# Kernel tuning notes

Measured on AMD Instinct MI355X. Metric: run time of the kernel, lower is better.

The kernel has to match this reference:

```python
import jax, jax.numpy as jnp
import numpy as np

N = 200000
C = 128
B = 4
HF, WF = 32, 88
IMG_H, IMG_W = 256, 704
STRIDE = 8
MAX_BEV_RANGE = 54.0
HID = max(C // 2, 32)
LN_EPS = 1e-5


def setup_inputs() -> dict:
    key = jax.random.key(0)
    ks = jax.random.split(key, 16)
    x = jax.random.normal(ks[0], (N, C), jnp.float32)
    bid = jax.random.randint(ks[1], (N, 1), 0, B)
    zi = jax.random.randint(ks[2], (N, 1), 0, 5)
    yi = jax.random.randint(ks[3], (N, 1), 0, 180)
    xi = jax.random.randint(ks[4], (N, 1), 0, 180)
    indices = jnp.concatenate([bid, zi, yi, xi], axis=1).astype(jnp.int32)
    voxel_size = jnp.array([0.075, 0.075, 0.2], jnp.float32)
    pc_range = jnp.array([-54.0, -54.0, -5.0, 54.0, 54.0, 3.0], jnp.float32)
    aug = jnp.tile(jnp.eye(4, dtype=jnp.float32)[None], (B, 1, 1)) + 0.01 * jax.random.normal(ks[5], (B, 4, 4), jnp.float32)
    # realistic pinhole lidar->image projection (depth = lidar +x)
    trans_base = np.array([[352.0, -560.0, 0.0, 0.0],
                           [128.0, 0.0, -560.0, 0.0],
                           [1.0, 0.0, 0.0, 0.0]], np.float32)
    trans = jnp.asarray(trans_base)[None] + 0.01 * jax.random.normal(ks[6], (B, 3, 4), jnp.float32)
    img_feats = jax.random.normal(ks[7], (B, C, HF, WF), jnp.float32)
    s = 0.05
    return {
        'x': x, 'indices': indices, 'voxel_size': voxel_size, 'pc_range': pc_range,
        'lidar_aug_matrix': aug, 'trans_lidar_to_img': trans, 'img_feats': img_feats,
        'W1_fg': s * jax.random.normal(ks[8], (C, HID), jnp.float32),
        'b1_fg': jnp.zeros((HID,), jnp.float32),
        'W2_fg': s * jax.random.normal(ks[9], (HID, 1), jnp.float32),
        'b2_fg': jnp.zeros((1,), jnp.float32),
        'We1': s * jax.random.normal(ks[10], (2 * C, C), jnp.float32),
        'be1': jnp.zeros((C,), jnp.float32),
        'We2': s * jax.random.normal(ks[11], (C, C), jnp.float32),
        'be2': jnp.zeros((C,), jnp.float32),
        'ln_gamma': jnp.ones((C,), jnp.float32),
        'ln_beta': jnp.zeros((C,), jnp.float32),
        'img_h': IMG_H, 'img_w': IMG_W,
    }


def _bilinear_gather(img_feats, batch_ids, u_norm, v_norm):
    # F.grid_sample(align_corners=True, padding_mode='zeros'), batched via per-point gather
    _, _, H, W = img_feats.shape
    xp = (u_norm + 1.0) * 0.5 * (W - 1)
    yp = (v_norm + 1.0) * 0.5 * (H - 1)
    x0 = jnp.floor(xp)
    y0 = jnp.floor(yp)
    wx1 = xp - x0
    wy1 = yp - y0

    def corner(xi, yi):
        ok = (xi >= 0) & (xi <= W - 1) & (yi >= 0) & (yi <= H - 1)
        xc = jnp.clip(xi, 0, W - 1).astype(jnp.int32)
        yc = jnp.clip(yi, 0, H - 1).astype(jnp.int32)
        return img_feats[batch_ids, :, yc, xc] * ok[:, None]  # [N, C]

    f00 = corner(x0, y0)
    f01 = corner(x0 + 1, y0)
    f10 = corner(x0, y0 + 1)
    f11 = corner(x0 + 1, y0 + 1)
    w00 = ((1 - wx1) * (1 - wy1))[:, None]
    w01 = (wx1 * (1 - wy1))[:, None]
    w10 = ((1 - wx1) * wy1)[:, None]
    w11 = (wx1 * wy1)[:, None]
    return w00 * f00 + w01 * f01 + w10 * f10 + w11 * f11


def reference(x, indices, voxel_size, pc_range, lidar_aug_matrix, trans_lidar_to_img, img_feats,
              W1_fg, b1_fg, W2_fg, b2_fg, We1, be1, We2, be2, ln_gamma, ln_beta, img_h, img_w):
    bids = indices[:, 0].astype(jnp.int32)
    # voxel centers: indices cols (z,y,x) -> (x,y,z)
    spatial = indices[:, jnp.array([3, 2, 1])].astype(jnp.float32)
    cvs = voxel_size * STRIDE
    centers = spatial * cvs + pc_range[:3] + cvs * 0.5  # [N, 3]
    range_norm = jnp.linalg.norm(centers[:, :2], axis=-1, keepdims=True)
    range_norm = jnp.clip(range_norm / max(MAX_BEV_RANGE, 1e-6), 0.0, 1.0)

    xyz_hom = jnp.concatenate([centers, jnp.ones((centers.shape[0], 1), centers.dtype)], axis=1)
    aug_inv = jnp.linalg.inv(lidar_aug_matrix)[bids]  # [N, 4, 4]
    xyz_hom = jnp.einsum('nij,nj->ni', aug_inv, xyz_hom)
    pts = jnp.einsum('nij,nj->ni', trans_lidar_to_img[bids], xyz_hom)  # [N, 3]
    depth = pts[:, 2]
    safe_depth = jnp.maximum(depth, 1e-5)
    u_img = pts[:, 0] / safe_depth
    v_img = pts[:, 1] / safe_depth
    Hf, Wf = img_feats.shape[2], img_feats.shape[3]
    u_norm = 2.0 * (u_img * (float(Wf) / float(img_w))) / max(Wf - 1, 1) - 1.0
    v_norm = 2.0 * (v_img * (float(Hf) / float(img_h))) / max(Hf - 1, 1) - 1.0
    valid = (depth > 1e-5) & (jnp.abs(u_norm) <= 1.0) & (jnp.abs(v_norm) <= 1.0)  # [N]
    valid_f = valid.astype(x.dtype)[:, None]

    sampled_img = _bilinear_gather(img_feats, bids, u_norm, v_norm)  # [N, C]

    # ForegroundHead
    p_fg = jax.nn.sigmoid(jax.nn.relu(x @ W1_fg + b1_fg) @ W2_fg + b2_fg)
    # ConventionalFusionExpert with projection-valid mask
    h = jax.nn.relu(jnp.concatenate([x, sampled_img], axis=-1) @ We1 + be1)
    delta = (h @ We2 + be2) * valid_f

    gain = jnp.linalg.norm(delta, axis=-1, keepdims=True) / (jnp.linalg.norm(x, axis=-1, keepdims=True) + 1e-6)
    fusion_gain = jnp.clip(1.0 - jnp.exp(-gain), 0.0, 1.0)

    xr = x + delta
    mu = jnp.mean(xr, axis=-1, keepdims=True)
    var = jnp.mean(jnp.square(xr - mu), axis=-1, keepdims=True)
    x_out = (xr - mu) * jax.lax.rsqrt(var + LN_EPS) * ln_gamma + ln_beta

    return (x_out, p_fg, fusion_gain, range_norm, valid_f)
```

## Files before the change

kernel.cpp:

```cpp
#include <hip/hip_runtime.h>
#include <math.h>

#define CD  128
#define HFD 32
#define WFD 88

typedef __attribute__((ext_vector_type(4))) float  f4;
typedef __attribute__((ext_vector_type(8))) __bf16 b8;

__device__ __forceinline__ f4 mfma16(b8 a, b8 b, f4 c) {
  return __builtin_amdgcn_mfma_f32_16x16x32_bf16(a, b, c, 0, 0, 0);
}

__global__ void prep_inv_kernel(const float* __restrict__ aug,
                                float* __restrict__ auginv, int B) {
  int b = threadIdx.x;
  if (b >= B) return;
  double m[4][8];
  for (int i = 0; i < 4; ++i)
    for (int j = 0; j < 4; ++j) {
      m[i][j]     = (double)aug[b * 16 + i * 4 + j];
      m[i][4 + j] = (i == j) ? 1.0 : 0.0;
    }
  for (int col = 0; col < 4; ++col) {
    int piv = col;
    double best = fabs(m[col][col]);
    for (int r = col + 1; r < 4; ++r) {
      double v = fabs(m[r][col]);
      if (v > best) { best = v; piv = r; }
    }
    if (piv != col)
      for (int j = 0; j < 8; ++j) {
        double t = m[col][j]; m[col][j] = m[piv][j]; m[piv][j] = t;
      }
    double f = 1.0 / m[col][col];
    for (int j = 0; j < 8; ++j) m[col][j] *= f;
    for (int r = 0; r < 4; ++r)
      if (r != col) {
        double gg = m[r][col];
        for (int j = 0; j < 8; ++j) m[r][j] -= gg * m[col][j];
      }
  }
  for (int i = 0; i < 4; ++i)
    for (int j = 0; j < 4; ++j)
      auginv[b * 16 + i * 4 + j] = (float)m[i][4 + j];
}

__global__ void transpose_img_kernel(const float* __restrict__ img,
                                     __bf16* __restrict__ imgT, int total) {
  int o = blockIdx.x * blockDim.x + threadIdx.x;
  if (o >= total) return;
  int c   = o & (CD - 1);
  int pos = o >> 7;
  int xw  = pos % WFD;
  int tmp = pos / WFD;
  int yh  = tmp & (HFD - 1);
  int b   = tmp >> 5;
  imgT[o] = (__bf16)img[((b * CD + c) * HFD + yh) * WFD + xw];
}

__global__ void pack_weights_kernel(const float* __restrict__ W1,
                                    const float* __restrict__ We1,
                                    const float* __restrict__ We2,
                                    short* __restrict__ W1t,
                                    short* __restrict__ We1t,
                                    short* __restrict__ We2t) {
  int i = blockIdx.x * 256 + threadIdx.x;
  const float* W; short* O; int KB, Nw, idx; bool cmap;
  if (i < 8192)       { W = W1;  O = W1t;  KB = 4; Nw = 64;  idx = i;         cmap = true;  }
  else if (i < 40960) { W = We1; O = We1t; KB = 8; Nw = 128; idx = i - 8192;  cmap = true;  }
  else if (i < 57344) { W = We2; O = We2t; KB = 4; Nw = 128; idx = i - 40960; cmap = false; }
  else return;
  const int j    = idx & 7;
  const int lane = (idx >> 3) & 63;
  const int blk  = idx >> 9;
  const int kb   = blk % KB, mb = blk / KB;
  const int ch   = 16 * mb + (lane & 15);
  const int k    = cmap ? (32 * kb + 8 * (lane >> 4) + j)
                        : (32 * kb + 4 * (lane >> 4) + (j & 3) + 16 * (j >> 2));
  __bf16 h = (__bf16)W[k * Nw + ch];
  short s;
  __builtin_memcpy(&s, &h, 2);
  O[idx] = s;
}

__device__ __forceinline__ void geo_cat(
    int nc, int g, const float* __restrict__ x,
    const int* __restrict__ indices, const __bf16* __restrict__ imgT,
    const float* __restrict__ auginv, const float* __restrict__ trans,
    float vsx, float vsy, float vsz, float pcx, float pcy, float pcz,
    float su, float sv, b8* catf, float& vf_o, float& rn_o) {
  const int4 idx = *reinterpret_cast<const int4*>(indices + (size_t)nc * 4);
  const int  b   = idx.x;
  const float cx = (float)idx.w * vsx + pcx + 0.5f * vsx;
  const float cy = (float)idx.z * vsy + pcy + 0.5f * vsy;
  const float cz = (float)idx.y * vsz + pcz + 0.5f * vsz;

  const f4 A0 = *reinterpret_cast<const f4*>(auginv + b * 16 + 0);
  const f4 A1 = *reinterpret_cast<const f4*>(auginv + b * 16 + 4);
  const f4 A2 = *reinterpret_cast<const f4*>(auginv + b * 16 + 8);
  const f4 A3 = *reinterpret_cast<const f4*>(auginv + b * 16 + 12);
  const float h0 = A0[0] * cx + A0[1] * cy + A0[2] * cz + A0[3];
  const float h1 = A1[0] * cx + A1[1] * cy + A1[2] * cz + A1[3];
  const float h2 = A2[0] * cx + A2[1] * cy + A2[2] * cz + A2[3];
  const float h3 = A3[0] * cx + A3[1] * cy + A3[2] * cz + A3[3];
  const f4 T0 = *reinterpret_cast<const f4*>(trans + b * 12 + 0);
  const f4 T1 = *reinterpret_cast<const f4*>(trans + b * 12 + 4);
  const f4 T2 = *reinterpret_cast<const f4*>(trans + b * 12 + 8);
  const float q0    = T0[0] * h0 + T0[1] * h1 + T0[2] * h2 + T0[3] * h3;
  const float q1    = T1[0] * h0 + T1[1] * h1 + T1[2] * h2 + T1[3] * h3;
  const float depth = T2[0] * h0 + T2[1] * h1 + T2[2] * h2 + T2[3] * h3;
  const float safe  = fmaxf(depth, 1e-5f);
  const float u = q0 / safe, v = q1 / safe;
  const float un = 2.0f * (u * su) / 87.0f - 1.0f;
  const float vn = 2.0f * (v * sv) / 31.0f - 1.0f;
  vf_o = (depth > 1e-5f && fabsf(un) <= 1.0f && fabsf(vn) <= 1.0f) ? 1.0f : 0.0f;
  float rn = sqrtf(cx * cx + cy * cy) / 54.0f;
  rn_o = fminf(fmaxf(rn, 0.0f), 1.0f);

  const float xp  = (un + 1.0f) * 0.5f * 87.0f;
  const float yp  = (vn + 1.0f) * 0.5f * 31.0f;
  const float x0f = floorf(xp), y0f = floorf(yp);
  const float wx1 = xp - x0f, wy1 = yp - y0f;
  const float wx0 = 1.0f - wx1, wy0 = 1.0f - wy1;
  const bool okx0 = (x0f >= 0.0f) && (x0f <= 87.0f);
  const bool okx1 = (x0f + 1.0f >= 0.0f) && (x0f + 1.0f <= 87.0f);
  const bool oky0 = (y0f >= 0.0f) && (y0f <= 31.0f);
  const bool oky1 = (y0f + 1.0f >= 0.0f) && (y0f + 1.0f <= 31.0f);
  const int ix0 = (int)fminf(fmaxf(x0f, 0.0f), 87.0f);
  const int ix1 = (int)fminf(fmaxf(x0f + 1.0f, 0.0f), 87.0f);
  const int iy0 = (int)fminf(fmaxf(y0f, 0.0f), 31.0f);
  const int iy1 = (int)fminf(fmaxf(y0f + 1.0f, 0.0f), 31.0f);
  const float w00 = (okx0 && oky0) ? (wx0 * wy0) : 0.0f;
  const float w01 = (okx1 && oky0) ? (wx1 * wy0) : 0.0f;
  const float w10 = (okx0 && oky1) ? (wx0 * wy1) : 0.0f;
  const float w11 = (okx1 && oky1) ? (wx1 * wy1) : 0.0f;
  const int o00 = (iy0 * WFD + ix0) * CD;
  const int o01 = (iy0 * WFD + ix1) * CD;
  const int o10 = (iy1 * WFD + ix0) * CD;
  const int o11 = (iy1 * WFD + ix1) * CD;
  const __bf16* ib = imgT + (size_t)b * (HFD * WFD * CD);

  const float* xr = x + (size_t)nc * CD + 8 * g;
#pragma unroll
  for (int kb = 0; kb < 4; ++kb) {
    const f4 a = *reinterpret_cast<const f4*>(xr + 32 * kb);
    const f4 c = *reinterpret_cast<const f4*>(xr + 32 * kb + 4);
    b8 t;
#pragma unroll
    for (int e = 0; e < 4; ++e) {
      t[e]     = (__bf16)a[e];
      t[4 + e] = (__bf16)c[e];
    }
    catf[kb] = t;
  }
#pragma unroll
  for (int kb = 0; kb < 4; ++kb) {
    const int off = 32 * kb + 8 * g;
    const b8 f00 = *reinterpret_cast<const b8*>(ib + o00 + off);
    const b8 f01 = *reinterpret_cast<const b8*>(ib + o01 + off);
    const b8 f10 = *reinterpret_cast<const b8*>(ib + o10 + off);
    const b8 f11 = *reinterpret_cast<const b8*>(ib + o11 + off);
    b8 t;
#pragma unroll
    for (int e = 0; e < 8; ++e) {
      const float s = w00 * (float)f00[e] + w01 * (float)f01[e] +
                      w10 * (float)f10[e] + w11 * (float)f11[e];
      t[e] = (__bf16)s;
    }
    catf[4 + kb] = t;
  }
}

__device__ __forceinline__ void epilogue_pt(
    const f4* acc3, float vf, float rn, float sfg, int n, int nc, int g, int N,
    const float* __restrict__ x, const float* __restrict__ lng,
    const float* __restrict__ lnb, const float* __restrict__ b2,
    float* __restrict__ out, size_t OFF_PFG, size_t OFF_GAIN, size_t OFF_RN,
    size_t OFF_VAL) {
  f4 xrv[8];
  float sd = 0.0f, sx2 = 0.0f, sr = 0.0f, sr2 = 0.0f;
#pragma unroll
  for (int mb = 0; mb < 8; ++mb) {
    const f4 xv = *reinterpret_cast<const f4*>(x + (size_t)nc * CD + 16 * mb + 4 * g);
    const f4 d  = acc3[mb] * vf;
    const f4 r  = xv + d;
    xrv[mb] = r;
#pragma unroll
    for (int e = 0; e < 4; ++e) {
      sd  += d[e] * d[e];
      sx2 += xv[e] * xv[e];
      sr  += r[e];
      sr2 += r[e] * r[e];
    }
  }
  sd  += __shfl_xor(sd, 16);  sd  += __shfl_xor(sd, 32);
  sx2 += __shfl_xor(sx2, 16); sx2 += __shfl_xor(sx2, 32);
  sr  += __shfl_xor(sr, 16);  sr  += __shfl_xor(sr, 32);
  sr2 += __shfl_xor(sr2, 16); sr2 += __shfl_xor(sr2, 32);

  const float mu   = sr * (1.0f / 128.0f);
  const float var  = sr2 * (1.0f / 128.0f) - mu * mu;
  const float rstd = rsqrtf(var + 1e-5f);
  const float gn   = sqrtf(sd) / (sqrtf(sx2) + 1e-6f);
  const float fgain = fminf(fmaxf(1.0f - expf(-gn), 0.0f), 1.0f);

  if (n < N) {
#pragma unroll
    for (int mb = 0; mb < 8; ++mb) {
      const f4 gm = *reinterpret_cast<const f4*>(lng + 16 * mb + 4 * g);
      const f4 bt = *reinterpret_cast<const f4*>(lnb + 16 * mb + 4 * g);
      const f4 o  = (xrv[mb] - mu) * rstd * gm + bt;
      *reinterpret_cast<f4*>(out + (size_t)n * CD + 16 * mb + 4 * g) = o;
    }
    if (g == 0) {
      out[OFF_PFG  + n] = 1.0f / (1.0f + expf(-(sfg + b2[0])));
      out[OFF_GAIN + n] = fgain;
      out[OFF_RN   + n] = rn;
      out[OFF_VAL  + n] = vf;
    }
  }
}

__global__ __launch_bounds__(256)
void fused_mfma_kernel(const float* __restrict__ x,
                       const int* __restrict__ indices,
                       const float* __restrict__ voxel_size,
                       const float* __restrict__ pc_range,
                       const float* __restrict__ trans,
                       const float* __restrict__ auginv,
                       const __bf16* __restrict__ imgT,
                       const __bf16* __restrict__ W1t,
                       const float* __restrict__ b1,
                       const float* __restrict__ W2,
                       const float* __restrict__ b2,
                       const __bf16* __restrict__ We1t,
                       const float* __restrict__ be1,
                       const __bf16* __restrict__ We2t,
                       const float* __restrict__ be2,
                       const float* __restrict__ lng,
                       const float* __restrict__ lnb,
                       const int* __restrict__ img_h_p,
                       const int* __restrict__ img_w_p,
                       float* __restrict__ out, int N) {
  const int lane = threadIdx.x & 63;
  const int wv   = threadIdx.x >> 6;
  const int g    = lane >> 4;
  const int pl   = lane & 15;
  const int n0   = blockIdx.x * 128 + wv * 32 + pl;
  const int n1   = n0 + 16;
  const int nc0  = (n0 < N) ? n0 : (N - 1);
  const int nc1  = (n1 < N) ? n1 : (N - 1);

  const size_t NN       = (size_t)N;
  const size_t OFF_PFG  = NN * CD;
  const size_t OFF_GAIN = OFF_PFG + NN;
  const size_t OFF_RN   = OFF_GAIN + NN;
  const size_t OFF_VAL  = OFF_RN + NN;

  const float vsx = voxel_size[0] * 8.0f;
  const float vsy = voxel_size[1] * 8.0f;
  const float vsz = voxel_size[2] * 8.0f;
  const float pcx = pc_range[0], pcy = pc_range[1], pcz = pc_range[2];
  const float su  = (float)WFD / (float)(*img_w_p);
  const float sv  = (float)HFD / (float)(*img_h_p);

  b8 cat0[8], cat1[8];
  float vf0, rn0, vf1, rn1;
  geo_cat(nc0, g, x, indices, imgT, auginv, trans, vsx, vsy, vsz,
          pcx, pcy, pcz, su, sv, cat0, vf0, rn0);
  geo_cat(nc1, g, x, indices, imgT, auginv, trans, vsx, vsy, vsz,
          pcx, pcy, pcz, su, sv, cat1, vf1, rn1);

  float sfg0 = 0.0f, sfg1 = 0.0f;
#pragma unroll
  for (int mb = 0; mb < 4; ++mb) {
    const f4 bi = *reinterpret_cast<const f4*>(b1 + 16 * mb + 4 * g);
    f4 a0 = bi, a1 = bi;
#pragma unroll
    for (int kb = 0; kb < 4; ++kb) {
      const b8 w = *reinterpret_cast<const b8*>(
          W1t + ((size_t)(mb * 4 + kb) * 64 + lane) * 8);
      a0 = mfma16(w, cat0[kb], a0);
      a1 = mfma16(w, cat1[kb], a1);
    }
    const f4 w2v = *reinterpret_cast<const f4*>(W2 + 16 * mb + 4 * g);
#pragma unroll
    for (int e = 0; e < 4; ++e) {
      sfg0 += fmaxf(a0[e], 0.0f) * w2v[e];
      sfg1 += fmaxf(a1[e], 0.0f) * w2v[e];
    }
  }
  sfg0 += __shfl_xor(sfg0, 16); sfg0 += __shfl_xor(sfg0, 32);
  sfg1 += __shfl_xor(sfg1, 16); sfg1 += __shfl_xor(sfg1, 32);

  b8 b30[4], b31[4];
#pragma unroll
  for (int pr = 0; pr < 4; ++pr) {
    const f4 biA = *reinterpret_cast<const f4*>(be1 + 16 * (2 * pr) + 4 * g);
    const f4 biB = *reinterpret_cast<const f4*>(be1 + 16 * (2 * pr + 1) + 4 * g);
    f4 aA0 = biA, aB0 = biB, aA1 = biA, aB1 = biB;
#pragma unroll
    for (int kb = 0; kb < 8; ++kb) {
      const b8 wA = *reinterpret_cast<const b8*>(
          We1t + ((size_t)((2 * pr) * 8 + kb) * 64 + lane) * 8);
      const b8 wB = *reinterpret_cast<const b8*>(
          We1t + ((size_t)((2 * pr + 1) * 8 + kb) * 64 + lane) * 8);
      aA0 = mfma16(wA, cat0[kb], aA0);
      aB0 = mfma16(wB, cat0[kb], aB0);
      aA1 = mfma16(wA, cat1[kb], aA1);
      aB1 = mfma16(wB, cat1[kb], aB1);
    }
    b8 t0, t1;
#pragma unroll
    for (int e = 0; e < 4; ++e) {
      t0[e]     = (__bf16)fmaxf(aA0[e], 0.0f);
      t0[4 + e] = (__bf16)fmaxf(aB0[e], 0.0f);
      t1[e]     = (__bf16)fmaxf(aA1[e], 0.0f);
      t1[4 + e] = (__bf16)fmaxf(aB1[e], 0.0f);
    }
    b30[pr] = t0;
    b31[pr] = t1;
  }

  f4 acc30[8], acc31[8];
#pragma unroll
  for (int mb = 0; mb < 8; ++mb) {
    const f4 bi = *reinterpret_cast<const f4*>(be2 + 16 * mb + 4 * g);
    acc30[mb] = bi;
    acc31[mb] = bi;
  }
#pragma unroll
  for (int kb = 0; kb < 4; ++kb) {
#pragma unroll
    for (int mb = 0; mb < 8; ++mb) {
      const b8 w = *reinterpret_cast<const b8*>(
          We2t + ((size_t)(mb * 4 + kb) * 64 + lane) * 8);
      acc30[mb] = mfma16(w, b30[kb], acc30[mb]);
      acc31[mb] = mfma16(w, b31[kb], acc31[mb]);
    }
  }

  epilogue_pt(acc30, vf0, rn0, sfg0, n0, nc0, g, N, x, lng, lnb, b2, out,
              OFF_PFG, OFF_GAIN, OFF_RN, OFF_VAL);
  epilogue_pt(acc31, vf1, rn1, sfg1, n1, nc1, g, N, x, lng, lnb, b2, out,
              OFF_PFG, OFF_GAIN, OFF_RN, OFF_VAL);
}

extern "C" void kernel_launch(void* const* d_in, const int* in_sizes, int n_in,
                              void* d_out, int out_size, void* d_ws, size_t ws_size,
                              hipStream_t stream) {
  const float* x       = (const float*)d_in[0];
  const int*   indices = (const int*)d_in[1];
  const float* voxel   = (const float*)d_in[2];
  const float* pcr     = (const float*)d_in[3];
  const float* aug     = (const float*)d_in[4];
  const float* trans   = (const float*)d_in[5];
  const float* img     = (const float*)d_in[6];
  const float* W1      = (const float*)d_in[7];
  const float* b1      = (const float*)d_in[8];
  const float* W2      = (const float*)d_in[9];
  const float* b2      = (const float*)d_in[10];
  const float* We1     = (const float*)d_in[11];
  const float* be1     = (const float*)d_in[12];
  const float* We2     = (const float*)d_in[13];
  const float* be2     = (const float*)d_in[14];
  const float* lng     = (const float*)d_in[15];
  const float* lnb     = (const float*)d_in[16];
  const int*   img_h   = (const int*)d_in[17];
  const int*   img_w   = (const int*)d_in[18];

  const int N         = in_sizes[0] / CD;
  const int B         = in_sizes[4] / 16;
  const int img_total = in_sizes[6];
  const size_t IMG_BYTES = (size_t)img_total * 2;

  char*   wsb    = (char*)d_ws;
  float*  auginv = (float*)wsb;
  __bf16* imgT   = (__bf16*)(wsb + 1024);
  short*  W1t    = (short*)(wsb + 1024 + IMG_BYTES);
  short*  We1t   = W1t + 8192;
  short*  We2t   = We1t + 32768;

  prep_inv_kernel<<<1, 64, 0, stream>>>(aug, auginv, B);
  transpose_img_kernel<<<(img_total + 255) / 256, 256, 0, stream>>>(
      img, imgT, img_total);
  pack_weights_kernel<<<224, 256, 0, stream>>>(W1, We1, We2, W1t, We1t, We2t);
  fused_mfma_kernel<<<(N + 127) / 128, 256, 0, stream>>>(
      x, indices, voxel, pcr, trans, auginv, imgT,
      (const __bf16*)W1t, b1, W2, b2,
      (const __bf16*)We1t, be1,
      (const __bf16*)We2t, be2,
      lng, lnb, img_h, img_w, (float*)d_out, N);
}
```

Before: 133.6 us.

## Stage packed MLP weights in LDS and use 768-thread blocks with one point-tile per wave

The fused kernel now copies all packed bf16 weights (W1, We1, We2, about 112 KB) into shared memory at block start, and the MFMA loops read weight fragments from LDS instead of global memory. Blocks grow to 768 threads covering 192 points, with each wave handling a single 16-point tile instead of two, which lowers register pressure. The aim is to cut repeated global/L2 weight traffic and raise occupancy. The cost is a large per-block LDS fill plus a barrier, and 112 KB of LDS per block limits how many blocks fit on each CU.

```diff
diff --git a/kernel.cpp b/kernel.cpp
--- a/kernel.cpp
+++ b/kernel.cpp
@@ -222,7 +222,7 @@
   }
 }
 
-__global__ __launch_bounds__(256)
+__global__ __launch_bounds__(768)
 void fused_mfma_kernel(const float* __restrict__ x,
                        const int* __restrict__ indices,
                        const float* __restrict__ voxel_size,
@@ -230,33 +230,49 @@
                        const float* __restrict__ trans,
                        const float* __restrict__ auginv,
                        const __bf16* __restrict__ imgT,
-                       const __bf16* __restrict__ W1t,
+                       const short* __restrict__ wsrc,
                        const float* __restrict__ b1,
                        const float* __restrict__ W2,
                        const float* __restrict__ b2,
-                       const __bf16* __restrict__ We1t,
                        const float* __restrict__ be1,
-                       const __bf16* __restrict__ We2t,
                        const float* __restrict__ be2,
                        const float* __restrict__ lng,
                        const float* __restrict__ lnb,
                        const int* __restrict__ img_h_p,
                        const int* __restrict__ img_w_p,
                        float* __restrict__ out, int N) {
-  const int lane = threadIdx.x & 63;
-  const int wv   = threadIdx.x >> 6;
+  __shared__ __align__(16) short wlds[57344];
+  const int tid  = threadIdx.x;
+  const int lane = tid & 63;
+  const int wv   = tid >> 6;
   const int g    = lane >> 4;
   const int pl   = lane & 15;
-  const int n0   = blockIdx.x * 128 + wv * 32 + pl;
-  const int n1   = n0 + 16;
-  const int nc0  = (n0 < N) ? n0 : (N - 1);
-  const int nc1  = (n1 < N) ? n1 : (N - 1);
+  const int n    = blockIdx.x * 192 + wv * 16 + pl;
+  const int nc   = (n < N) ? n : (N - 1);
 
   const size_t NN       = (size_t)N;
   const size_t OFF_PFG  = NN * CD;
   const size_t OFF_GAIN = OFF_PFG + NN;
   const size_t OFF_RN   = OFF_GAIN + NN;
   const size_t OFF_VAL  = OFF_RN + NN;
+
+  {
+    const uint4* ws4 = reinterpret_cast<const uint4*>(wsrc);
+    uint4* wl4       = reinterpret_cast<uint4*>(wlds);
+    uint4 tmp[10];
+#pragma unroll
+    for (int i = 0; i < 10; ++i) {
+      int c = tid + i * 768;
+      if (c >= 7168) c -= 7168;
+      tmp[i] = ws4[c];
+    }
+#pragma unroll
+    for (int i = 0; i < 10; ++i) {
+      int c = tid + i * 768;
+      if (c >= 7168) c -= 7168;
+      wl4[c] = tmp[i];
+    }
+  }
 
   const float vsx = voxel_size[0] * 8.0f;
   const float vsy = voxel_size[1] * 8.0f;
@@ -265,85 +281,66 @@
   const float su  = (float)WFD / (float)(*img_w_p);
   const float sv  = (float)HFD / (float)(*img_h_p);
 
-  b8 cat0[8], cat1[8];
-  float vf0, rn0, vf1, rn1;
-  geo_cat(nc0, g, x, indices, imgT, auginv, trans, vsx, vsy, vsz,
-          pcx, pcy, pcz, su, sv, cat0, vf0, rn0);
-  geo_cat(nc1, g, x, indices, imgT, auginv, trans, vsx, vsy, vsz,
-          pcx, pcy, pcz, su, sv, cat1, vf1, rn1);
-
-  float sfg0 = 0.0f, sfg1 = 0.0f;
+  b8 cat[8];
+  float vf, rn;
+  geo_cat(nc, g, x, indices, imgT, auginv, trans, vsx, vsy, vsz,
+          pcx, pcy, pcz, su, sv, cat, vf, rn);
+
+  __syncthreads();
+
+  const short* wb = wlds + lane * 8;
+
+  float sfg = 0.0f;
 #pragma unroll
   for (int mb = 0; mb < 4; ++mb) {
-    const f4 bi = *reinterpret_cast<const f4*>(b1 + 16 * mb + 4 * g);
-    f4 a0 = bi, a1 = bi;
+    f4 a = *reinterpret_cast<const f4*>(b1 + 16 * mb + 4 * g);
 #pragma unroll
     for (int kb = 0; kb < 4; ++kb) {
-      const b8 w = *reinterpret_cast<const b8*>(
-          W1t + ((size_t)(mb * 4 + kb) * 64 + lane) * 8);
-      a0 = mfma16(w, cat0[kb], a0);
-      a1 = mfma16(w, cat1[kb], a1);
+      const b8 w = *reinterpret_cast<const b8*>(wb + (mb * 4 + kb) * 512);
+      a = mfma16(w, cat[kb], a);
     }
     const f4 w2v = *reinterpret_cast<const f4*>(W2 + 16 * mb + 4 * g);
 #pragma unroll
+    for (int e = 0; e < 4; ++e) sfg += fmaxf(a[e], 0.0f) * w2v[e];
+  }
+  sfg += __shfl_xor(sfg, 16);
+  sfg += __shfl_xor(sfg, 32);
+
+  b8 b3[4];
+#pragma unroll
+  for (int pr = 0; pr < 4; ++pr) {
+    f4 aA = *reinterpret_cast<const f4*>(be1 + 16 * (2 * pr) + 4 * g);
+    f4 aB = *reinterpret_cast<const f4*>(be1 + 16 * (2 * pr + 1) + 4 * g);
+#pragma unroll
+    for (int kb = 0; kb < 8; ++kb) {
+      const b8 wA = *reinterpret_cast<const b8*>(wb + (16 + (2 * pr) * 8 + kb) * 512);
+      const b8 wB = *reinterpret_cast<const b8*>(wb + (16 + (2 * pr + 1) * 8 + kb) * 512);
+      aA = mfma16(wA, cat[kb], aA);
+      aB = mfma16(wB, cat[kb], aB);
+    }
+    b8 t;
+#pragma unroll
     for (int e = 0; e < 4; ++e) {
-      sfg0 += fmaxf(a0[e], 0.0f) * w2v[e];
-      sfg1 += fmaxf(a1[e], 0.0f) * w2v[e];
-    }
-  }
-  sfg0 += __shfl_xor(sfg0, 16); sfg0 += __shfl_xor(sfg0, 32);
-  sfg1 += __shfl_xor(sfg1, 16); sfg1 += __shfl_xor(sfg1, 32);
-
-  b8 b30[4], b31[4];
-#pragma unroll
-  for (int pr = 0; pr < 4; ++pr) {
-    const f4 biA = *reinterpret_cast<const f4*>(be1 + 16 * (2 * pr) + 4 * g);
-    const f4 biB = *reinterpret_cast<const f4*>(be1 + 16 * (2 * pr + 1) + 4 * g);
-    f4 aA0 = biA, aB0 = biB, aA1 = biA, aB1 = biB;
-#pragma unroll
-    for (int kb = 0; kb < 8; ++kb) {
-      const b8 wA = *reinterpret_cast<const b8*>(
-          We1t + ((size_t)((2 * pr) * 8 + kb) * 64 + lane) * 8);
-      const b8 wB = *reinterpret_cast<const b8*>(
-          We1t + ((size_t)((2 * pr + 1) * 8 + kb) * 64 + lane) * 8);
-      aA0 = mfma16(wA, cat0[kb], aA0);
-      aB0 = mfma16(wB, cat0[kb], aB0);
-      aA1 = mfma16(wA, cat1[kb], aA1);
-      aB1 = mfma16(wB, cat1[kb], aB1);
-    }
-    b8 t0, t1;
-#pragma unroll
-    for (int e = 0; e < 4; ++e) {
-      t0[e]     = (__bf16)fmaxf(aA0[e], 0.0f);
-      t0[4 + e] = (__bf16)fmaxf(aB0[e], 0.0f);
-      t1[e]     = (__bf16)fmaxf(aA1[e], 0.0f);
-      t1[4 + e] = (__bf16)fmaxf(aB1[e], 0.0f);
-    }
-    b30[pr] = t0;
-    b31[pr] = t1;
-  }
-
-  f4 acc30[8], acc31[8];
-#pragma unroll
-  for (int mb = 0; mb < 8; ++mb) {
-    const f4 bi = *reinterpret_cast<const f4*>(be2 + 16 * mb + 4 * g);
-    acc30[mb] = bi;
-    acc31[mb] = bi;
-  }
+      t[e]     = (__bf16)fmaxf(aA[e], 0.0f);
+      t[4 + e] = (__bf16)fmaxf(aB[e], 0.0f);
+    }
+    b3[pr] = t;
+  }
+
+  f4 acc3[8];
+#pragma unroll
+  for (int mb = 0; mb < 8; ++mb)
+    acc3[mb] = *reinterpret_cast<const f4*>(be2 + 16 * mb + 4 * g);
 #pragma unroll
   for (int kb = 0; kb < 4; ++kb) {
 #pragma unroll
     for (int mb = 0; mb < 8; ++mb) {
-      const b8 w = *reinterpret_cast<const b8*>(
-          We2t + ((size_t)(mb * 4 + kb) * 64 + lane) * 8);
-      acc30[mb] = mfma16(w, b30[kb], acc30[mb]);
-      acc31[mb] = mfma16(w, b31[kb], acc31[mb]);
-    }
-  }
-
-  epilogue_pt(acc30, vf0, rn0, sfg0, n0, nc0, g, N, x, lng, lnb, b2, out,
-              OFF_PFG, OFF_GAIN, OFF_RN, OFF_VAL);
-  epilogue_pt(acc31, vf1, rn1, sfg1, n1, nc1, g, N, x, lng, lnb, b2, out,
+      const b8 w = *reinterpret_cast<const b8*>(wb + (80 + mb * 4 + kb) * 512);
+      acc3[mb] = mfma16(w, b3[kb], acc3[mb]);
+    }
+  }
+
+  epilogue_pt(acc3, vf, rn, sfg, n, nc, g, N, x, lng, lnb, b2, out,
               OFF_PFG, OFF_GAIN, OFF_RN, OFF_VAL);
 }
 
@@ -386,10 +383,8 @@
   transpose_img_kernel<<<(img_total + 255) / 256, 256, 0, stream>>>(
       img, imgT, img_total);
   pack_weights_kernel<<<224, 256, 0, stream>>>(W1, We1, We2, W1t, We1t, We2t);
-  fused_mfma_kernel<<<(N + 127) / 128, 256, 0, stream>>>(
+  fused_mfma_kernel<<<(N + 191) / 192, 768, 0, stream>>>(
       x, indices, voxel, pcr, trans, auginv, imgT,
-      (const __bf16*)W1t, b1, W2, b2,
-      (const __bf16*)We1t, be1,
-      (const __bf16*)We2t, be2,
+      W1t, b1, W2, b2, be1, be2,
       lng, lnb, img_h, img_w, (float*)d_out, N);
 }
```

Result: faster. 120.7 us (-9.7%).

## Stage packed MLP weights in LDS via async global_load_lds with larger blocks

Applied to the files above, without the earlier changes.

The fused kernel now copies all packed bf16 weight fragments (W1, We1, We2; 112 KB) into shared memory using async global-to-LDS loads issued before the geometry/gather phase, so the copy overlaps that work. MFMA weight operands then come from LDS instead of per-wave global/L2 reads. Blocks grow from 256 to 768 threads (384 points each) to amortize the staging cost. The large LDS footprint limits occupancy to one block per CU, and each block pays a barrier before compute.

```diff
diff --git a/kernel.cpp b/kernel.cpp
--- a/kernel.cpp
+++ b/kernel.cpp
@@ -222,7 +222,7 @@
   }
 }
 
-__global__ __launch_bounds__(256)
+__global__ __launch_bounds__(768)
 void fused_mfma_kernel(const float* __restrict__ x,
                        const int* __restrict__ indices,
                        const float* __restrict__ voxel_size,
@@ -230,24 +230,24 @@
                        const float* __restrict__ trans,
                        const float* __restrict__ auginv,
                        const __bf16* __restrict__ imgT,
-                       const __bf16* __restrict__ W1t,
+                       const short* __restrict__ wsrc,
                        const float* __restrict__ b1,
                        const float* __restrict__ W2,
                        const float* __restrict__ b2,
-                       const __bf16* __restrict__ We1t,
                        const float* __restrict__ be1,
-                       const __bf16* __restrict__ We2t,
                        const float* __restrict__ be2,
                        const float* __restrict__ lng,
                        const float* __restrict__ lnb,
                        const int* __restrict__ img_h_p,
                        const int* __restrict__ img_w_p,
                        float* __restrict__ out, int N) {
-  const int lane = threadIdx.x & 63;
-  const int wv   = threadIdx.x >> 6;
+  __shared__ __align__(16) short wlds[57344];
+  const int tid  = threadIdx.x;
+  const int lane = tid & 63;
+  const int wv   = tid >> 6;
   const int g    = lane >> 4;
   const int pl   = lane & 15;
-  const int n0   = blockIdx.x * 128 + wv * 32 + pl;
+  const int n0   = blockIdx.x * 384 + wv * 32 + pl;
   const int n1   = n0 + 16;
   const int nc0  = (n0 < N) ? n0 : (N - 1);
   const int nc1  = (n1 < N) ? n1 : (N - 1);
@@ -257,6 +257,18 @@
   const size_t OFF_GAIN = OFF_PFG + NN;
   const size_t OFF_RN   = OFF_GAIN + NN;
   const size_t OFF_VAL  = OFF_RN + NN;
+
+#pragma unroll
+  for (int i = 0; i < 10; ++i) {
+    const int f = wv + i * 12;
+    if (f < 112) {
+      __builtin_amdgcn_global_load_lds(
+          (const __attribute__((address_space(1))) unsigned int*)
+              (wsrc + (size_t)f * 512 + lane * 8),
+          (__attribute__((address_space(3))) unsigned int*)(wlds + f * 512),
+          16, 0, 0);
+    }
+  }
 
   const float vsx = voxel_size[0] * 8.0f;
   const float vsy = voxel_size[1] * 8.0f;
@@ -272,6 +284,10 @@
   geo_cat(nc1, g, x, indices, imgT, auginv, trans, vsx, vsy, vsz,
           pcx, pcy, pcz, su, sv, cat1, vf1, rn1);
 
+  __syncthreads();
+
+  const short* wb = wlds + lane * 8;
+
   float sfg0 = 0.0f, sfg1 = 0.0f;
 #pragma unroll
   for (int mb = 0; mb < 4; ++mb) {
@@ -279,8 +295,7 @@
     f4 a0 = bi, a1 = bi;
 #pragma unroll
     for (int kb = 0; kb < 4; ++kb) {
-      const b8 w = *reinterpret_cast<const b8*>(
-          W1t + ((size_t)(mb * 4 + kb) * 64 + lane) * 8);
+      const b8 w = *reinterpret_cast<const b8*>(wb + (mb * 4 + kb) * 512);
       a0 = mfma16(w, cat0[kb], a0);
       a1 = mfma16(w, cat1[kb], a1);
     }
@@ -302,10 +317,8 @@
     f4 aA0 = biA, aB0 = biB, aA1 = biA, aB1 = biB;
 #pragma unroll
     for (int kb = 0; kb < 8; ++kb) {
-      const b8 wA = *reinterpret_cast<const b8*>(
-          We1t + ((size_t)((2 * pr) * 8 + kb) * 64 + lane) * 8);
-      const b8 wB = *reinterpret_cast<const b8*>(
-          We1t + ((size_t)((2 * pr + 1) * 8 + kb) * 64 + lane) * 8);
+      const b8 wA = *reinterpret_cast<const b8*>(wb + (16 + (2 * pr) * 8 + kb) * 512);
+      const b8 wB = *reinterpret_cast<const b8*>(wb + (16 + (2 * pr + 1) * 8 + kb) * 512);
       aA0 = mfma16(wA, cat0[kb], aA0);
       aB0 = mfma16(wB, cat0[kb], aB0);
       aA1 = mfma16(wA, cat1[kb], aA1);
@@ -334,8 +347,7 @@
   for (int kb = 0; kb < 4; ++kb) {
 #pragma unroll
     for (int mb = 0; mb < 8; ++mb) {
-      const b8 w = *reinterpret_cast<const b8*>(
-          We2t + ((size_t)(mb * 4 + kb) * 64 + lane) * 8);
+      const b8 w = *reinterpret_cast<const b8*>(wb + (80 + mb * 4 + kb) * 512);
       acc30[mb] = mfma16(w, b30[kb], acc30[mb]);
       acc31[mb] = mfma16(w, b31[kb], acc31[mb]);
     }
@@ -386,10 +398,8 @@
   transpose_img_kernel<<<(img_total + 255) / 256, 256, 0, stream>>>(
       img, imgT, img_total);
   pack_weights_kernel<<<224, 256, 0, stream>>>(W1, We1, We2, W1t, We1t, We2t);
-  fused_mfma_kernel<<<(N + 127) / 128, 256, 0, stream>>>(
+  fused_mfma_kernel<<<(N + 383) / 384, 768, 0, stream>>>(
       x, indices, voxel, pcr, trans, auginv, imgT,
-      (const __bf16*)W1t, b1, W2, b2,
-      (const __bf16*)We1t, be1,
-      (const __bf16*)We2t, be2,
+      W1t, b1, W2, b2, be1, be2,
       lng, lnb, img_h, img_w, (float*)d_out, N);
 }
```

Result: slower. 139.0 us (+4.0%).
